# Kernel optimization log

Measured on AMD Instinct MI355X. Metric: run time of the kernel, lower is better.

Reference implementation:

```python
import jax, jax.numpy as jnp
import numpy as np

N = 16384      # total nodes in batched graph
E = 131072     # message-passing edges
E_RO = 32768   # readout edges
D = 1024       # fc7 appearance feature dim
DL = 300       # word2vec dim
DS = 16        # spatial edge feature dim
C = 117        # HICO verb classes


def setup_inputs() -> dict:
    key = jax.random.key(0)
    ks = jax.random.split(key, 20)
    s = 0.02
    return {
        'feat': jax.random.normal(ks[0], (N, D), jnp.float32),
        'word2vec': jax.random.normal(ks[1], (N, DL), jnp.float32),
        's_f': jax.random.normal(ks[2], (E, DS), jnp.float32),
        's_f_ro': jax.random.normal(ks[3], (E_RO, DS), jnp.float32),
        'W_e': jax.random.normal(ks[4], (2 * D + DS, D), jnp.float32) * s,
        'b_e': jnp.zeros((D,), jnp.float32),
        'W_el': jax.random.normal(ks[5], (2 * DL, DL), jnp.float32) * s,
        'b_el': jnp.zeros((DL,), jnp.float32),
        'W_nu': jax.random.normal(ks[6], (2 * D, D), jnp.float32) * s,
        'b_nu': jnp.zeros((D,), jnp.float32),
        'W_nul': jax.random.normal(ks[7], (2 * DL, DL), jnp.float32) * s,
        'b_nul': jnp.zeros((DL,), jnp.float32),
        'W_p': jax.random.normal(ks[8], (D + DL + DS + DL + D, C), jnp.float32) * s,
        'b_p': jnp.zeros((C,), jnp.float32),
        'edge_src': jax.random.randint(ks[9], (E,), 0, N, jnp.int32),
        'edge_dst': jax.random.randint(ks[10], (E,), 0, N, jnp.int32),
        'ro_src': jax.random.randint(ks[11], (E_RO,), 0, N, jnp.int32),
        'ro_dst': jax.random.randint(ks[12], (E_RO,), 0, N, jnp.int32),
    }


def _mean_agg(msgs, dst, n, dtype):
    # scatter-add messages to destination nodes, then mean-normalize
    summed = jax.ops.segment_sum(msgs, dst, num_segments=n)
    cnt = jax.ops.segment_sum(jnp.ones((msgs.shape[0], 1), dtype), dst, num_segments=n)
    return summed / jnp.maximum(cnt, 1.0)


def reference(feat, word2vec, s_f, s_f_ro, W_e, b_e, W_el, b_el,
              W_nu, b_nu, W_nul, b_nul, W_p, b_p,
              edge_src, edge_dst, ro_src, ro_dst):
    # --- GRNN message passing: gather -> concat -> MLP -> scatter(mean) ---
    # appearance stream: [src_feat, dst_feat, s_f] -> relu(MLP)
    m = jax.nn.relu(
        jnp.concatenate([feat[edge_src], feat[edge_dst], s_f], axis=1) @ W_e + b_e)
    agg = _mean_agg(m, edge_dst, N, feat.dtype)               # [N, D]
    # language stream: [src_w2v, dst_w2v] -> relu(MLP)
    ml = jax.nn.relu(
        jnp.concatenate([word2vec[edge_src], word2vec[edge_dst]], axis=1) @ W_el + b_el)
    aggl = _mean_agg(ml, edge_dst, N, feat.dtype)             # [N, DL]

    # --- NodeUpdate: concat(original, aggregated) -> MLP ---
    new_n_f = jax.nn.relu(jnp.concatenate([feat, agg], axis=1) @ W_nu + b_nu)
    new_n_f_lang = jax.nn.relu(
        jnp.concatenate([word2vec, aggl], axis=1) @ W_nul + b_nul)

    # --- Predictor (edge readout): concat[dst_f, dst_lang, s_f, src_lang, src_f] ---
    ef = jnp.concatenate([
        new_n_f[ro_dst], new_n_f_lang[ro_dst], s_f_ro,
        new_n_f_lang[ro_src], new_n_f[ro_src]], axis=1)       # [E_RO, 2664]
    pred = ef @ W_p + b_p                                     # [E_RO, 117]
    return pred
```

## Files before the change

kernel.cpp:

```cpp
#include <hip/hip_runtime.h>

typedef unsigned short u16;
typedef __attribute__((ext_vector_type(8))) short short8;
typedef __attribute__((ext_vector_type(4))) float f32x4;

#define NN 16384
#define EE 131072
#define ERO 32768
#define DF 1024
#define DL 300
#define DLP 320
#define DLN 384
#define DS 16
#define NC 117
#define NCP 128

__device__ __forceinline__ float bf2f(u16 x) {
  unsigned int u = ((unsigned int)x) << 16;
  float f;
  __builtin_memcpy(&f, &u, 4);
  return f;
}
__device__ __forceinline__ u16 f2bf(float f) {
  unsigned int u;
  __builtin_memcpy(&u, &f, 4);
  u = (u + 0x7FFFu + ((u >> 16) & 1u)) >> 16;
  return (u16)u;
}
__device__ __forceinline__ float ld1(const void* p, size_t i, int f) {
  return f ? ((const float*)p)[i] : bf2f(((const u16*)p)[i]);
}
__device__ __forceinline__ void ld4(const void* p, size_t i, int f,
                                    float& x, float& y, float& z, float& w) {
  if (f) {
    float4 v = *(const float4*)((const float*)p + i);
    x = v.x; y = v.y; z = v.z; w = v.w;
  } else {
    ushort4 v = *(const ushort4*)((const u16*)p + i);
    x = bf2f(v.x); y = bf2f(v.y); z = bf2f(v.z); w = bf2f(v.w);
  }
}
__device__ __forceinline__ const void* eoff(const void* p, size_t off, int f) {
  return f ? (const void*)((const float*)p + off) : (const void*)((const u16*)p + off);
}

__global__ void detect_kernel(const unsigned int* __restrict__ w, int* __restrict__ flag) {
  unsigned int x = w[threadIdx.x];
  int e = (x >> 7) & 0xFF;
  int ok = (e >= 97 && e <= 157);
  unsigned long long m = __ballot(ok);
  if (threadIdx.x == 0) flag[0] = (__popcll(m) >= 48) ? 0 : 1;
}

__global__ void cast_bf16(const int* __restrict__ flag, const void* __restrict__ src,
                          u16* __restrict__ dst, int total8) {
  const int i = blockIdx.x * 256 + threadIdx.x;
  if (i >= total8) return;
  const int fin = flag[0];
  const size_t o = (size_t)i * 8;
  float x0, x1, x2, x3, x4, x5, x6, x7;
  ld4(src, o, fin, x0, x1, x2, x3);
  ld4(src, o + 4, fin, x4, x5, x6, x7);
  ushort4 lo, hi;
  lo.x = f2bf(x0); lo.y = f2bf(x1); lo.z = f2bf(x2); lo.w = f2bf(x3);
  hi.x = f2bf(x4); hi.y = f2bf(x5); hi.z = f2bf(x6); hi.w = f2bf(x7);
  *(ushort4*)(dst + o) = lo;
  *(ushort4*)(dst + o + 4) = hi;
}

struct TJob2 {
  const void* W; long off;
  u16* out;
  int Kr, Nr, Nstr, Kp, Np, blk0;
};
struct TPack2 { TJob2 j[12]; int nj; };

__global__ void prep_weights2(const int* __restrict__ flag, TPack2 P) {
  int b = blockIdx.x;
  int ji = 0;
  while (ji + 1 < P.nj && b >= P.j[ji + 1].blk0) ++ji;
  const TJob2 J = P.j[ji];
  const int idx = (b - J.blk0) * 256 + threadIdx.x;
  if (idx >= J.Np * J.Kp) return;
  const int n = idx / J.Kp, k = idx % J.Kp;
  float v = 0.f;
  if (k < J.Kr && n < J.Nr) v = ld1(J.W, (size_t)J.off + (size_t)k * J.Nstr + n, flag[0]);
  J.out[idx] = f2bf(v);
}

__device__ __forceinline__ void stage_bf16_async(const u16* __restrict__ G, size_t rbase,
                                                 int lda, int k0, u16* lds, int w, int lane) {
  #pragma unroll
  for (int t = 0; t < 2; ++t) {
    const int rr = (w << 5) + (t << 4) + (lane >> 2);
    const u16* gp = G + (rbase + rr) * (size_t)lda + k0 + ((lane & 3) << 3);
    __builtin_amdgcn_global_load_lds(
        (const __attribute__((address_space(1))) void*)gp,
        (__attribute__((address_space(3))) void*)(lds + (((w << 5) + (t << 4)) * 32)),
        16, 0, 0);
  }
}

__device__ __forceinline__ void stage_f32_manual(const float* __restrict__ G, int row0,
                                                 int lda, int k0, int Kreal,
                                                 u16* lds, int tid) {
  const int r = tid >> 1, half = tid & 1;
  const float* gp = G + (size_t)(row0 + r) * lda + k0 + (half << 4);
  #pragma unroll
  for (int qq = 0; qq < 4; ++qq) {
    const int kk = k0 + (half << 4) + (qq << 2);
    float4 v = make_float4(0.f, 0.f, 0.f, 0.f);
    if (kk < Kreal) v = *(const float4*)(gp + (qq << 2));
    ushort4 o;
    o.x = f2bf(v.x); o.y = f2bf(v.y); o.z = f2bf(v.z); o.w = f2bf(v.w);
    *(ushort4*)(lds + r * 32 + (half << 4) + (qq << 2)) = o;
  }
}

__device__ __forceinline__ void kloop(int am, const void* __restrict__ A, int lda,
                                      int Kreal, int Kpad, const u16* __restrict__ B,
                                      u16* As, u16* Bs, f32x4 (&acc)[4][4],
                                      int row0, int col0,
                                      int tid, int lane, int w, int wm, int wn, int ml, int q) {
  for (int k0 = 0; k0 < Kpad; k0 += 32) {
    if (am == 0) stage_bf16_async((const u16*)A, (size_t)row0, lda, k0, As, w, lane);
    else         stage_f32_manual((const float*)A, row0, lda, k0, Kreal, As, tid);
    stage_bf16_async(B, (size_t)col0, Kpad, k0, Bs, w, lane);
    __syncthreads();
    short8 af[4], bfr[4];
    #pragma unroll
    for (int i = 0; i < 4; ++i)
      af[i] = *(const short8*)(As + ((wm << 6) + (i << 4) + ml) * 32 + (q << 3));
    #pragma unroll
    for (int j = 0; j < 4; ++j)
      bfr[j] = *(const short8*)(Bs + ((wn << 6) + (j << 4) + ml) * 32 + (q << 3));
    #pragma unroll
    for (int i = 0; i < 4; ++i)
      #pragma unroll
      for (int j = 0; j < 4; ++j)
        acc[i][j] = __builtin_amdgcn_mfma_f32_16x16x32_bf16(af[i], bfr[j], acc[i][j], 0, 0, 0);
    __syncthreads();
  }
}

struct GJob {
  const void* A1; const u16* B1;
  const void* A2; const u16* B2;
  const void* bias; void* C;
  int lda1, K1real, K1pad, am1;
  int lda2, K2real, K2pad, am2;
  int inBias, ldc, Nreal, Npad, relu, cf32;
  int gx, gy, blk0;
};
struct GPack { GJob j[2]; int nj; };

__global__ __launch_bounds__(256) void mfma_jobs(const int* __restrict__ flag, GPack P) {
  const int b = blockIdx.x;
  int ji = 0;
  if (P.nj > 1 && b >= P.j[1].blk0) ji = 1;
  const GJob J = P.j[ji];
  const int t = b - J.blk0;
  const int xcd = t & 7, s = t >> 3;
  const int row_t = xcd * (J.gy >> 3) + s / J.gx;
  const int col_t = s % J.gx;
  const int row0 = row_t << 7;
  const int col0 = col_t << 7;

  __shared__ __attribute__((aligned(16))) u16 As[128 * 32];
  __shared__ __attribute__((aligned(16))) u16 Bs[128 * 32];
  const int tid = threadIdx.x;
  const int lane = tid & 63;
  const int w = tid >> 6;
  const int wm = w >> 1, wn = w & 1;
  const int ml = lane & 15, q = lane >> 4;

  f32x4 acc[4][4];
  #pragma unroll
  for (int i = 0; i < 4; ++i)
    #pragma unroll
    for (int j = 0; j < 4; ++j) {
      f32x4 z = {0.f, 0.f, 0.f, 0.f};
      acc[i][j] = z;
    }

  kloop(J.am1, J.A1, J.lda1, J.K1real, J.K1pad, J.B1, As, Bs, acc,
        row0, col0, tid, lane, w, wm, wn, ml, q);
  if (J.am2 >= 0)
    kloop(J.am2, J.A2, J.lda2, J.K2real, J.K2pad, J.B2, As, Bs, acc,
          row0, col0, tid, lane, w, wm, wn, ml, q);

  const int fin = flag[0];
  #pragma unroll
  for (int j = 0; j < 4; ++j) {
    const int col = col0 + (wn << 6) + (j << 4) + ml;
    if (col >= J.Npad) continue;
    float bv = 0.f;
    if (J.bias && col < J.Nreal) bv = ld1(J.bias, col, J.inBias ? fin : 0);
    #pragma unroll
    for (int i = 0; i < 4; ++i) {
      #pragma unroll
      for (int r = 0; r < 4; ++r) {
        const int row = row0 + (wm << 6) + (i << 4) + (q << 2) + r;
        float v = 0.f;
        if (col < J.Nreal) {
          v = acc[i][j][r] + bv;
          if (J.relu) v = fmaxf(v, 0.f);
        }
        if (J.cf32) ((float*)J.C)[(size_t)row * J.ldc + col] = v;
        else        ((u16*)J.C)[(size_t)row * J.ldc + col] = f2bf(v);
      }
    }
  }
}


struct G2Job {
  const u16* A1; const u16* B1;
  const u16* A2; const u16* B2;
  const void* bias; u16* C;
  int ldk;
  int nt1, nt2;
  int gx;
  int ldc, Nreal, relu, inBias;
};

#define L2_HALF 16384
#define L2_BUF  65536

__device__ __forceinline__ void barrier_f() {
  asm volatile("" ::: "memory");
  __builtin_amdgcn_s_barrier();
  asm volatile("" ::: "memory");
}

__device__ __forceinline__ void read4f(const char* base, short8 (&dst)[4]) {
  #pragma unroll
  for (int i = 0; i < 4; ++i) dst[i] = *(const short8*)(base + i * 1024);
}

__device__ __forceinline__ void mfma16(f32x4 (&acc)[8][4], const short8 (&af)[4],
                                       const short8 (&bfr)[4], int mg) {
  __builtin_amdgcn_s_setprio(1);
  #pragma unroll
  for (int i = 0; i < 4; ++i)
    #pragma unroll
    for (int n = 0; n < 4; ++n)
      acc[mg * 4 + i][n] =
          __builtin_amdgcn_mfma_f32_16x16x32_bf16(af[i], bfr[n], acc[mg * 4 + i][n], 0, 0, 0);
  __builtin_amdgcn_s_setprio(0);
}

__global__ __launch_bounds__(512, 2) void mfma256(const int* __restrict__ flag, G2Job J) {
  __shared__ __attribute__((aligned(16))) u16 LDS[65536];
  char* ldsc = (char*)LDS;

  const int nwg = gridDim.x;
  const int bid = blockIdx.x;
  const int wg = (bid & 7) * (nwg >> 3) + (bid >> 3);
  const int rt = wg / J.gx, ct = wg % J.gx;
  const int row0 = rt << 8, col0 = ct << 8;

  const int tid = threadIdx.x;
  const int lane = tid & 63, w = tid >> 6;
  const int wm = w >> 2, wn = w & 3;
  const int q = lane >> 4, ml = lane & 15;
  const int ldk = J.ldk;
  const int nt = J.nt1 + J.nt2;

  const int swzr = (ml * 64 + q * 16) ^ (((ml >> 1) & 3) << 4);
  const int ub = (lane * 16) ^ (((lane >> 3) & 3) << 4);
  const int r_in = ub >> 6, c_in = (ub & 63) >> 1;

  f32x4 acc[8][4];
  #pragma unroll
  for (int m = 0; m < 8; ++m)
    #pragma unroll
    for (int n = 0; n < 4; ++n) { f32x4 z = {0.f, 0.f, 0.f, 0.f}; acc[m][n] = z; }

  auto stage = [&](int cb2, const u16* __restrict__ G, int rb, int kc, int boff, int kh) {
    char* lb = ldsc + cb2 * L2_BUF + boff + kh * L2_HALF + w * 2048;
    const u16* g0 = G + (size_t)(rb + w * 32 + r_in) * (size_t)ldk + kc;
    __builtin_amdgcn_global_load_lds((const __attribute__((address_space(1))) void*)g0,
        (__attribute__((address_space(3))) void*)lb, 16, 0, 0);
    const u16* g1 = g0 + (size_t)16 * ldk;
    __builtin_amdgcn_global_load_lds((const __attribute__((address_space(1))) void*)g1,
        (__attribute__((address_space(3))) void*)(lb + 1024), 16, 0, 0);
  };

  stage(0, J.A1, row0, 0 + c_in, 0, 0);
  stage(0, J.B1, col0, 0 + c_in, 32768, 0);
  stage(0, J.A1, row0, 32 + c_in, 0, 1);
  stage(0, J.B1, col0, 32 + c_in, 32768, 1);
  asm volatile("s_waitcnt vmcnt(4)" ::: "memory");
  barrier_f();

  int cb = 0;
  #pragma unroll 1
  for (int kt = 0; kt < nt; ++kt) {
    const int nk = (kt + 1 < nt) ? kt + 1 : kt;
    const u16* An = (nk < J.nt1) ? J.A1 : J.A2;
    const u16* Bn = (nk < J.nt1) ? J.B1 : J.B2;
    const int kb = ((nk < J.nt1) ? nk : nk - J.nt1) << 6;
    const char* abase = ldsc + cb * L2_BUF + wm * 8192 + swzr;
    const char* bbase = ldsc + cb * L2_BUF + 32768 + wn * 4096 + swzr;
    short8 a0[4], a1[4], bfr[4];

    read4f(abase, a0);
    read4f(bbase, bfr);
    stage(cb ^ 1, An, row0, kb + c_in, 0, 0);
    barrier_f();
    mfma16(acc, a0, bfr, 0);
    barrier_f();
    read4f(abase + 4096, a1);
    stage(cb ^ 1, Bn, col0, kb + c_in, 32768, 0);
    barrier_f();
    mfma16(acc, a1, bfr, 1);
    asm volatile("s_waitcnt vmcnt(4)" ::: "memory");
    barrier_f();
    read4f(abase + L2_HALF, a0);
    read4f(bbase + L2_HALF, bfr);
    stage(cb ^ 1, An, row0, kb + 32 + c_in, 0, 1);
    barrier_f();
    mfma16(acc, a0, bfr, 0);
    barrier_f();
    read4f(abase + L2_HALF + 4096, a1);
    stage(cb ^ 1, Bn, col0, kb + 32 + c_in, 32768, 1);
    barrier_f();
    mfma16(acc, a1, bfr, 1);
    asm volatile("s_waitcnt vmcnt(4)" ::: "memory");
    barrier_f();
    cb ^= 1;
  }

  const int fin = flag[0];
  #pragma unroll
  for (int n = 0; n < 4; ++n) {
    const int col = col0 + wn * 64 + n * 16 + ml;
    float bv = 0.f;
    if (J.bias && col < J.Nreal) bv = ld1(J.bias, col, J.inBias ? fin : 0);
    #pragma unroll
    for (int m = 0; m < 8; ++m) {
      #pragma unroll
      for (int r = 0; r < 4; ++r) {
        const int row = row0 + wm * 128 + m * 16 + q * 4 + r;
        float v = acc[m][n][r] + bv;
        if (J.relu) v = fmaxf(v, 0.f);
        J.C[(size_t)row * J.ldc + col] = f2bf(v);
      }
    }
  }
}

__global__ void cnt_kernel(const int* __restrict__ edst, int* __restrict__ cnt) {
  const int i = blockIdx.x * 256 + threadIdx.x;
  if (i < EE) atomicAdd(&cnt[edst[i]], 1);
}

__global__ __launch_bounds__(1024) void scan_kernel(const int* __restrict__ cnt,
                                                    int* __restrict__ offs,
                                                    int* __restrict__ woffs) {
  __shared__ int part[1024];
  const int t = threadIdx.x;
  const int base = t * 16;
  int loc[16];
  int s = 0;
  #pragma unroll
  for (int i = 0; i < 16; ++i) { loc[i] = s; s += cnt[base + i]; }
  part[t] = s;
  __syncthreads();
  for (int off = 1; off < 1024; off <<= 1) {
    int v = (t >= off) ? part[t - off] : 0;
    __syncthreads();
    part[t] += v;
    __syncthreads();
  }
  const int chunk_excl = (t == 0) ? 0 : part[t - 1];
  #pragma unroll
  for (int i = 0; i < 16; ++i) {
    int o = chunk_excl + loc[i];
    offs[base + i] = o;
    woffs[base + i] = o;
  }
  if (t == 1023) offs[NN] = part[1023];
}

__global__ void scatter_kernel(const int* __restrict__ esrc, const int* __restrict__ edst,
                               int* __restrict__ woffs,
                               int* __restrict__ order, int* __restrict__ srcs) {
  const int e = blockIdx.x * 256 + threadIdx.x;
  if (e < EE) {
    const int d = edst[e];
    const int pos = atomicAdd(&woffs[d], 1);
    order[pos] = e;
    srcs[pos] = esrc[e];
  }
}

__global__ __launch_bounds__(256) void app_agg(
    const int* __restrict__ flag,
    const u16* __restrict__ P12, const void* __restrict__ s_f,
    const void* __restrict__ W_eb, const void* __restrict__ b_e,
    const int* __restrict__ offs, const int* __restrict__ order,
    const int* __restrict__ srcs, u16* __restrict__ aggn)
{
  const int fin = flag[0];
  const int n = blockIdx.x;
  const int tid = threadIdx.x;
  const int c4 = tid << 2;
  const void* W_es = eoff(W_eb, (size_t)2 * DF * DF, fin);

  float wx[16], wy[16], wz[16], ww[16];
  #pragma unroll
  for (int k = 0; k < 16; ++k)
    ld4(W_es, (size_t)k * DF + c4, fin, wx[k], wy[k], wz[k], ww[k]);

  float be0, be1, be2, be3;
  ld4(b_e, c4, fin, be0, be1, be2, be3);
  const ushort4 p2 = *(const ushort4*)(P12 + (size_t)n * 2048 + 1024 + c4);
  const float base0 = bf2f(p2.x) + be0;
  const float base1 = bf2f(p2.y) + be1;
  const float base2 = bf2f(p2.z) + be2;
  const float base3 = bf2f(p2.w) + be3;

  const int beg = offs[n], end = offs[n + 1];
  float a0 = 0.f, a1 = 0.f, a2 = 0.f, a3 = 0.f;
  int j = beg;
  for (; j + 4 <= end; j += 4) {
    int ee[4], ss[4];
    #pragma unroll
    for (int m = 0; m < 4; ++m) { ee[m] = order[j + m]; ss[m] = srcs[j + m]; }
    float u0[4], u1[4], u2[4], u3[4], sfv[4][16];
    #pragma unroll
    for (int m = 0; m < 4; ++m) {
      #pragma unroll
      for (int k = 0; k < 16; k += 4)
        ld4(s_f, (size_t)ee[m] * DS + k, fin,
            sfv[m][k], sfv[m][k + 1], sfv[m][k + 2], sfv[m][k + 3]);
      const ushort4 pm = *(const ushort4*)(P12 + (size_t)ss[m] * 2048 + c4);
      u0[m] = bf2f(pm.x) + base0;
      u1[m] = bf2f(pm.y) + base1;
      u2[m] = bf2f(pm.z) + base2;
      u3[m] = bf2f(pm.w) + base3;
    }
    #pragma unroll
    for (int k = 0; k < 16; ++k)
      #pragma unroll
      for (int m = 0; m < 4; ++m) {
        u0[m] = fmaf(sfv[m][k], wx[k], u0[m]);
        u1[m] = fmaf(sfv[m][k], wy[k], u1[m]);
        u2[m] = fmaf(sfv[m][k], wz[k], u2[m]);
        u3[m] = fmaf(sfv[m][k], ww[k], u3[m]);
      }
    #pragma unroll
    for (int m = 0; m < 4; ++m) {
      a0 += fmaxf(u0[m], 0.f); a1 += fmaxf(u1[m], 0.f);
      a2 += fmaxf(u2[m], 0.f); a3 += fmaxf(u3[m], 0.f);
    }
  }
  for (; j < end; ++j) {
    const int e = order[j], s = srcs[j];
    float sf[16];
    #pragma unroll
    for (int k = 0; k < 16; k += 4)
      ld4(s_f, (size_t)e * DS + k, fin, sf[k], sf[k + 1], sf[k + 2], sf[k + 3]);
    const ushort4 p1 = *(const ushort4*)(P12 + (size_t)s * 2048 + c4);
    float v0 = bf2f(p1.x) + base0;
    float v1 = bf2f(p1.y) + base1;
    float v2 = bf2f(p1.z) + base2;
    float v3 = bf2f(p1.w) + base3;
    #pragma unroll
    for (int k = 0; k < 16; ++k) {
      v0 = fmaf(sf[k], wx[k], v0);
      v1 = fmaf(sf[k], wy[k], v1);
      v2 = fmaf(sf[k], wz[k], v2);
      v3 = fmaf(sf[k], ww[k], v3);
    }
    a0 += fmaxf(v0, 0.f); a1 += fmaxf(v1, 0.f);
    a2 += fmaxf(v2, 0.f); a3 += fmaxf(v3, 0.f);
  }
  const float inv = 1.f / fmaxf((float)(end - beg), 1.f);
  ushort4 o;
  o.x = f2bf(a0 * inv); o.y = f2bf(a1 * inv);
  o.z = f2bf(a2 * inv); o.w = f2bf(a3 * inv);
  *(ushort4*)(aggn + (size_t)n * DF + c4) = o;
}

__global__ __launch_bounds__(320) void lang_agg(
    const int* __restrict__ flag,
    const u16* __restrict__ Q12, const void* __restrict__ b_el,
    const int* __restrict__ offs, const int* __restrict__ srcs,
    u16* __restrict__ aggln)
{
  const int fin = flag[0];
  const int n = blockIdx.x;
  const int c = threadIdx.x;
  if (c >= DL) { aggln[(size_t)n * DLP + c] = 0; return; }
  const float base = bf2f(Q12[(size_t)n * 768 + 384 + c]) + ld1(b_el, c, fin);
  const int beg = offs[n], end = offs[n + 1];
  float s0 = 0.f, s1 = 0.f, s2 = 0.f, s3 = 0.f;
  int j = beg;
  for (; j + 4 <= end; j += 4) {
    s0 += fmaxf(bf2f(Q12[(size_t)srcs[j] * 768 + c]) + base, 0.f);
    s1 += fmaxf(bf2f(Q12[(size_t)srcs[j + 1] * 768 + c]) + base, 0.f);
    s2 += fmaxf(bf2f(Q12[(size_t)srcs[j + 2] * 768 + c]) + base, 0.f);
    s3 += fmaxf(bf2f(Q12[(size_t)srcs[j + 3] * 768 + c]) + base, 0.f);
  }
  for (; j < end; ++j) s0 += fmaxf(bf2f(Q12[(size_t)srcs[j] * 768 + c]) + base, 0.f);
  const float a = (s0 + s1) + (s2 + s3);
  aggln[(size_t)n * DLP + c] = f2bf(a / fmaxf((float)(end - beg), 1.f));
}

__global__ __launch_bounds__(256) void readout_kernel(
    const int* __restrict__ flag,
    const float* __restrict__ RdRs,
    const void* __restrict__ s_f_ro,
    const void* __restrict__ W_pb, size_t offWps,
    const void* __restrict__ b_p,
    const int* __restrict__ rsrc, const int* __restrict__ rdst, void* __restrict__ out)
{
  const int fin = flag[0];
  __shared__ float wps[16 * NC];
  const void* Wp_s = eoff(W_pb, offWps, fin);
  const int tid = threadIdx.x;
  for (int i = tid; i < 16 * NC; i += 256) wps[i] = ld1(Wp_s, i, fin);
  __syncthreads();
  const int slot = tid >> 7;
  const int c = tid & 127;
  const float bp = (c < NC) ? ld1(b_p, c, fin) : 0.f;

  const int e0 = (blockIdx.x << 3) + slot;
  #pragma unroll
  for (int ee = 0; ee < 8; ee += 2) {
    const int e = e0 + ee;
    const int s = rsrc[e];
    const int d = rdst[e];
    if (c < NC) {
      float acc = RdRs[(size_t)d * 256 + c] + RdRs[(size_t)s * 256 + 128 + c] + bp;
      #pragma unroll
      for (int k = 0; k < 16; ++k)
        acc = fmaf(ld1(s_f_ro, (size_t)e * DS + k, fin), wps[k * NC + c], acc);
      if (fin) ((float*)out)[(size_t)e * NC + c] = acc;
      else     ((u16*)out)[(size_t)e * NC + c] = f2bf(acc);
    }
  }
}

extern "C" void kernel_launch(void* const* d_in, const int* in_sizes, int n_in,
                              void* d_out, int out_size, void* d_ws, size_t ws_size,
                              hipStream_t stream)
{
  const void* feat  = d_in[0];
  const void* w2v   = d_in[1];
  const void* s_f   = d_in[2];
  const void* s_fro = d_in[3];
  const void* W_e   = d_in[4];
  const void* b_e   = d_in[5];
  const void* W_el  = d_in[6];
  const void* b_el  = d_in[7];
  const void* W_nu  = d_in[8];
  const void* b_nu  = d_in[9];
  const void* W_nul = d_in[10];
  const void* b_nul = d_in[11];
  const void* W_p   = d_in[12];
  const void* b_p   = d_in[13];
  const int* esrc  = (const int*)d_in[14];
  const int* edst  = (const int*)d_in[15];
  const int* rsrc  = (const int*)d_in[16];
  const int* rdst  = (const int*)d_in[17];

  char* p = (char*)d_ws;
  int* flag  = (int*)p; p += 256;
  int* cnt   = (int*)p; p += (size_t)NN * 4;
  int* offs  = (int*)p; p += (size_t)(NN + 64) * 4;
  int* woffs = (int*)p; p += (size_t)NN * 4;
  int* order = (int*)p; p += (size_t)EE * 4;
  int* srcs  = (int*)p; p += (size_t)EE * 4;
  u16* featB  = (u16*)p; p += (size_t)NN * DF * 2;
  u16* We12T  = (u16*)p; p += (size_t)2 * DF * DF * 2;
  u16* Wnu1T  = (u16*)p; p += (size_t)DF * DF * 2;
  u16* Wnu2T  = (u16*)p; p += (size_t)DF * DF * 2;
  u16* Wel12T = (u16*)p; p += (size_t)2 * DLN * DLP * 2;
  u16* Wnul1T = (u16*)p; p += (size_t)DLN * DLP * 2;
  u16* Wnul2T = (u16*)p; p += (size_t)DLN * DLP * 2;
  u16* WpFT2  = (u16*)p; p += (size_t)2 * NCP * DF * 2;
  u16* WpLT2  = (u16*)p; p += (size_t)2 * NCP * DLP * 2;
  u16* P12   = (u16*)p; p += (size_t)NN * 2048 * 2;
  u16* Q12   = (u16*)p; p += (size_t)NN * 768 * 2;
  u16* aggln = (u16*)p; p += (size_t)NN * DLP * 2;
  u16* aggn  = (u16*)p; p += (size_t)NN * DF * 2;
  u16* newf = P12;
  u16* newl = P12 + (size_t)NN * DF;
  float* RdRs = (float*)Q12;

  detect_kernel<<<1, 64, 0, stream>>>((const unsigned int*)feat, flag);
  hipMemsetAsync(cnt, 0, (size_t)NN * 4, stream);
  cast_bf16<<<(NN * DF / 8 + 255) / 256, 256, 0, stream>>>(flag, feat, featB, NN * DF / 8);

  TPack2 tp{};
  int tb = 0, tn = 0;
  auto T = [&](const void* W, long off, int Kr, int Nr, int Nstr, u16* out, int Kp, int Np) {
    tp.j[tn] = TJob2{W, off, out, Kr, Nr, Nstr, Kp, Np, tb};
    tb += (Np * Kp + 255) / 256;
    ++tn;
  };
  T(W_e,   0,                   DF, DF, DF, We12T,                     DF, DF);
  T(W_e,   (long)DF * DF,       DF, DF, DF, We12T + (size_t)DF * DF,   DF, DF);
  T(W_nu,  0,                   DF, DF, DF, Wnu1T, DF, DF);
  T(W_nu,  (long)DF * DF,       DF, DF, DF, Wnu2T, DF, DF);
  T(W_el,  0,                   DL, DL, DL, Wel12T,                     DLP, DLN);
  T(W_el,  (long)DL * DL,       DL, DL, DL, Wel12T + (size_t)DLN * DLP, DLP, DLN);
  T(W_nul, 0,                   DL, DL, DL, Wnul1T, DLP, DLN);
  T(W_nul, (long)DL * DL,       DL, DL, DL, Wnul2T, DLP, DLN);
  T(W_p,   0,                                DF, NC, NC, WpFT2,                     DF,  NCP);
  T(W_p,   (long)(DF + DL + DS + DL) * NC,   DF, NC, NC, WpFT2 + (size_t)NCP * DF,  DF,  NCP);
  T(W_p,   (long)DF * NC,                    DL, NC, NC, WpLT2,                     DLP, NCP);
  T(W_p,   (long)(DF + DL + DS) * NC,        DL, NC, NC, WpLT2 + (size_t)NCP * DLP, DLP, NCP);
  tp.nj = tn;
  prep_weights2<<<tb, 256, 0, stream>>>(flag, tp);

  cnt_kernel<<<EE / 256, 256, 0, stream>>>(edst, cnt);
  scan_kernel<<<1, 1024, 0, stream>>>(cnt, offs, woffs);
  scatter_kernel<<<EE / 256, 256, 0, stream>>>(esrc, edst, woffs, order, srcs);

  {
    G2Job j{featB, We12T, nullptr, nullptr, nullptr, P12,
            DF, 16, 0, 8, 2048, 2048, 0, 0};
    mfma256<<<512, 512, 0, stream>>>(flag, j);
  }
  {
    GPack g{};
    g.j[0] = GJob{w2v, Wel12T, nullptr, nullptr, nullptr, Q12,
                  DL, DL, DLP, 1,   0, 0, 0, -1,
                  0, 768, 768, 768, 0, 0,    6, 128, 0};
    g.nj = 1;
    mfma_jobs<<<768, 256, 0, stream>>>(flag, g);
  }

  lang_agg<<<NN, DLP, 0, stream>>>(flag, Q12, b_el, offs, srcs, aggln);
  app_agg<<<NN, 256, 0, stream>>>(flag, P12, s_f, W_e, b_e, offs, order, srcs, aggn);

  {
    G2Job j{featB, Wnu1T, aggn, Wnu2T, b_nu, newf,
            DF, 16, 16, 4, DF, DF, 1, 1};
    mfma256<<<256, 512, 0, stream>>>(flag, j);
  }
  {
    GPack g{};
    g.j[0] = GJob{w2v, Wnul1T, aggln, Wnul2T, b_nul, newl,
                  DL, DL, DLP, 1,   DLP, DLP, DLP, 0,
                  1, DLP, DL, DLP, 1, 0,     3, 128, 0};
    g.nj = 1;
    mfma_jobs<<<384, 256, 0, stream>>>(flag, g);
  }

  {
    GPack g{};
    g.j[0] = GJob{newf, WpFT2, newl, WpLT2, nullptr, RdRs,
                  DF, DF, DF, 0,    DLP, DLP, DLP, 0,
                  0, 256, 256, 256, 0, 1,    2, 128, 0};
    g.nj = 1;
    mfma_jobs<<<256, 256, 0, stream>>>(flag, g);
  }

  readout_kernel<<<ERO / 8, 256, 0, stream>>>(flag, RdRs, s_fro,
                                              W_p, (size_t)(DF + DL) * NC, b_p,
                                              rsrc, rdst, d_out);
}
```

Before: 659.0 us.

## Batch language GEMMs into the 256-tile MFMA kernel with pre-cast word2vec

Word2vec is now cast once to padded bf16 so the language-stream GEMMs can run in the 256x256 MFMA kernel, which takes a two-job pack and runs them alongside the appearance GEMMs in a single launch. This removes separate generic-kernel launches and their tail underutilisation. Columns past the real width are written as zero or skipped. app_agg is also templated on the input-format flag and software-prefetches the next group's source rows. The trade-offs are an extra cast kernel and wasted work in the padded 256-wide tiles for the narrow 300/320-column problems.

```diff
diff --git a/kernel.cpp b/kernel.cpp
--- a/kernel.cpp
+++ b/kernel.cpp
@@ -68,6 +68,26 @@
   *(ushort4*)(dst + o + 4) = hi;
 }
 
+__global__ void cast_w2v(const int* __restrict__ flag, const void* __restrict__ src,
+                         u16* __restrict__ dst) {
+  const int i = blockIdx.x * 256 + threadIdx.x;
+  if (i >= NN * 80) return;
+  const int fin = flag[0];
+  const int n = i / 80, g = i - n * 80;
+  const int c = g << 2;
+  ushort4 o;
+  if (c < DL) {
+    const size_t base = (size_t)n * DL + c;
+    o.x = f2bf(ld1(src, base + 0, fin));
+    o.y = f2bf(ld1(src, base + 1, fin));
+    o.z = f2bf(ld1(src, base + 2, fin));
+    o.w = f2bf(ld1(src, base + 3, fin));
+  } else {
+    o.x = 0; o.y = 0; o.z = 0; o.w = 0;
+  }
+  *(ushort4*)(dst + (size_t)n * DLP + c) = o;
+}
+
 struct TJob2 {
   const void* W; long off;
   u16* out;
@@ -222,7 +242,9 @@
   int nt1, nt2;
   int gx;
   int ldc, Nreal, relu, inBias;
+  int nwg, blk0;
 };
+struct G2Pack { G2Job j[2]; int nj; };
 
 #define L2_HALF 16384
 #define L2_BUF  65536
@@ -250,13 +272,15 @@
   __builtin_amdgcn_s_setprio(0);
 }
 
-__global__ __launch_bounds__(512, 2) void mfma256(const int* __restrict__ flag, G2Job J) {
+__global__ __launch_bounds__(512, 2) void mfma256(const int* __restrict__ flag, G2Pack P) {
   __shared__ __attribute__((aligned(16))) u16 LDS[65536];
   char* ldsc = (char*)LDS;
 
-  const int nwg = gridDim.x;
   const int bid = blockIdx.x;
-  const int wg = (bid & 7) * (nwg >> 3) + (bid >> 3);
+  const int ji = (P.nj > 1 && bid >= P.j[1].blk0) ? 1 : 0;
+  const G2Job J = P.j[ji];
+  const int b = bid - J.blk0;
+  const int wg = (b & 7) * (J.nwg >> 3) + (b >> 3);
   const int rt = wg / J.gx, ct = wg % J.gx;
   const int row0 = rt << 8, col0 = ct << 8;
 
@@ -336,6 +360,7 @@
   #pragma unroll
   for (int n = 0; n < 4; ++n) {
     const int col = col0 + wn * 64 + n * 16 + ml;
+    if (col >= J.ldc) continue;
     float bv = 0.f;
     if (J.bias && col < J.Nreal) bv = ld1(J.bias, col, J.inBias ? fin : 0);
     #pragma unroll
@@ -343,8 +368,11 @@
       #pragma unroll
       for (int r = 0; r < 4; ++r) {
         const int row = row0 + wm * 128 + m * 16 + q * 4 + r;
-        float v = acc[m][n][r] + bv;
-        if (J.relu) v = fmaxf(v, 0.f);
+        float v = 0.f;
+        if (col < J.Nreal) {
+          v = acc[m][n][r] + bv;
+          if (J.relu) v = fmaxf(v, 0.f);
+        }
         J.C[(size_t)row * J.ldc + col] = f2bf(v);
       }
     }
@@ -396,27 +424,26 @@
   }
 }
 
-__global__ __launch_bounds__(256) void app_agg(
-    const int* __restrict__ flag,
+template<int FIN>
+__device__ __forceinline__ void app_agg_body(
     const u16* __restrict__ P12, const void* __restrict__ s_f,
     const void* __restrict__ W_eb, const void* __restrict__ b_e,
     const int* __restrict__ offs, const int* __restrict__ order,
     const int* __restrict__ srcs, u16* __restrict__ aggn)
 {
-  const int fin = flag[0];
   const int n = blockIdx.x;
   const int tid = threadIdx.x;
   const int c4 = tid << 2;
-  const void* W_es = eoff(W_eb, (size_t)2 * DF * DF, fin);
+  const void* W_es = eoff(W_eb, (size_t)2 * DF * DF, FIN);
 
   float wx[16], wy[16], wz[16], ww[16];
   #pragma unroll
   for (int k = 0; k < 16; ++k)
-    ld4(W_es, (size_t)k * DF + c4, fin, wx[k], wy[k], wz[k], ww[k]);
+    ld4(W_es, (size_t)k * DF + c4, FIN, wx[k], wy[k], wz[k], ww[k]);
 
   float be0, be1, be2, be3;
-  ld4(b_e, c4, fin, be0, be1, be2, be3);
-  const ushort4 p2 = *(const ushort4*)(P12 + (size_t)n * 2048 + 1024 + c4);
+  ld4(b_e, c4, FIN, be0, be1, be2, be3);
+  const ushort4 p2 = *(const ushort4*)(P12 + ((size_t)(unsigned)(n << 11)) + 1024 + c4);
   const float base0 = bf2f(p2.x) + be0;
   const float base1 = bf2f(p2.y) + be1;
   const float base2 = bf2f(p2.z) + be2;
@@ -425,22 +452,41 @@
   const int beg = offs[n], end = offs[n + 1];
   float a0 = 0.f, a1 = 0.f, a2 = 0.f, a3 = 0.f;
   int j = beg;
-  for (; j + 4 <= end; j += 4) {
-    int ee[4], ss[4];
-    #pragma unroll
-    for (int m = 0; m < 4; ++m) { ee[m] = order[j + m]; ss[m] = srcs[j + m]; }
+
+  int ee0[4];
+  ushort4 pm0[4];
+  if (j + 4 <= end) {
+    #pragma unroll
+    for (int m = 0; m < 4; ++m) {
+      ee0[m] = order[j + m];
+      const int ssm = srcs[j + m];
+      pm0[m] = *(const ushort4*)(P12 + ((size_t)(unsigned)(ssm << 11)) + c4);
+    }
+  }
+  for (; j + 4 <= end;) {
+    const int jn = j + 4;
+    const bool pref = (jn + 4 <= end);
+    int ee1[4];
+    ushort4 pm1[4];
+    if (pref) {
+      #pragma unroll
+      for (int m = 0; m < 4; ++m) {
+        ee1[m] = order[jn + m];
+        const int ssm = srcs[jn + m];
+        pm1[m] = *(const ushort4*)(P12 + ((size_t)(unsigned)(ssm << 11)) + c4);
+      }
+    }
     float u0[4], u1[4], u2[4], u3[4], sfv[4][16];
     #pragma unroll
     for (int m = 0; m < 4; ++m) {
       #pragma unroll
       for (int k = 0; k < 16; k += 4)
-        ld4(s_f, (size_t)ee[m] * DS + k, fin,
+        ld4(s_f, (size_t)ee0[m] * DS + k, FIN,
             sfv[m][k], sfv[m][k + 1], sfv[m][k + 2], sfv[m][k + 3]);
-      const ushort4 pm = *(const ushort4*)(P12 + (size_t)ss[m] * 2048 + c4);
-      u0[m] = bf2f(pm.x) + base0;
-      u1[m] = bf2f(pm.y) + base1;
-      u2[m] = bf2f(pm.z) + base2;
-      u3[m] = bf2f(pm.w) + base3;
+      u0[m] = bf2f(pm0[m].x) + base0;
+      u1[m] = bf2f(pm0[m].y) + base1;
+      u2[m] = bf2f(pm0[m].z) + base2;
+      u3[m] = bf2f(pm0[m].w) + base3;
     }
     #pragma unroll
     for (int k = 0; k < 16; ++k)
@@ -456,14 +502,19 @@
       a0 += fmaxf(u0[m], 0.f); a1 += fmaxf(u1[m], 0.f);
       a2 += fmaxf(u2[m], 0.f); a3 += fmaxf(u3[m], 0.f);
     }
+    j = jn;
+    if (pref) {
+      #pragma unroll
+      for (int m = 0; m < 4; ++m) { ee0[m] = ee1[m]; pm0[m] = pm1[m]; }
+    }
   }
   for (; j < end; ++j) {
     const int e = order[j], s = srcs[j];
     float sf[16];
     #pragma unroll
     for (int k = 0; k < 16; k += 4)
-      ld4(s_f, (size_t)e * DS + k, fin, sf[k], sf[k + 1], sf[k + 2], sf[k + 3]);
-    const ushort4 p1 = *(const ushort4*)(P12 + (size_t)s * 2048 + c4);
+      ld4(s_f, (size_t)e * DS + k, FIN, sf[k], sf[k + 1], sf[k + 2], sf[k + 3]);
+    const ushort4 p1 = *(const ushort4*)(P12 + ((size_t)(unsigned)(s << 11)) + c4);
     float v0 = bf2f(p1.x) + base0;
     float v1 = bf2f(p1.y) + base1;
     float v2 = bf2f(p1.z) + base2;
@@ -483,6 +534,17 @@
   o.x = f2bf(a0 * inv); o.y = f2bf(a1 * inv);
   o.z = f2bf(a2 * inv); o.w = f2bf(a3 * inv);
   *(ushort4*)(aggn + (size_t)n * DF + c4) = o;
+}
+
+__global__ __launch_bounds__(256) void app_agg(
+    const int* __restrict__ flag,
+    const u16* __restrict__ P12, const void* __restrict__ s_f,
+    const void* __restrict__ W_eb, const void* __restrict__ b_e,
+    const int* __restrict__ offs, const int* __restrict__ order,
+    const int* __restrict__ srcs, u16* __restrict__ aggn)
+{
+  if (flag[0]) app_agg_body<1>(P12, s_f, W_eb, b_e, offs, order, srcs, aggn);
+  else         app_agg_body<0>(P12, s_f, W_eb, b_e, offs, order, srcs, aggn);
 }
 
 __global__ __launch_bounds__(320) void lang_agg(
@@ -588,6 +650,7 @@
   u16* Q12   = (u16*)p; p += (size_t)NN * 768 * 2;
   u16* aggln = (u16*)p; p += (size_t)NN * DLP * 2;
   u16* aggn  = (u16*)p; p += (size_t)NN * DF * 2;
+  u16* w2vB  = (u16*)p; p += (size_t)NN * DLP * 2;
   u16* newf = P12;
   u16* newl = P12 + (size_t)NN * DF;
   float* RdRs = (float*)Q12;
@@ -595,6 +658,7 @@
   detect_kernel<<<1, 64, 0, stream>>>((const unsigned int*)feat, flag);
   hipMemsetAsync(cnt, 0, (size_t)NN * 4, stream);
   cast_bf16<<<(NN * DF / 8 + 255) / 256, 256, 0, stream>>>(flag, feat, featB, NN * DF / 8);
+  cast_w2v<<<(NN * 80 + 255) / 256, 256, 0, stream>>>(flag, w2v, w2vB);
 
   TPack2 tp{};
   int tb = 0, tn = 0;
@@ -623,34 +687,26 @@
   scatter_kernel<<<EE / 256, 256, 0, stream>>>(esrc, edst, woffs, order, srcs);
 
   {
-    G2Job j{featB, We12T, nullptr, nullptr, nullptr, P12,
-            DF, 16, 0, 8, 2048, 2048, 0, 0};
-    mfma256<<<512, 512, 0, stream>>>(flag, j);
-  }
-  {
-    GPack g{};
-    g.j[0] = GJob{w2v, Wel12T, nullptr, nullptr, nullptr, Q12,
-                  DL, DL, DLP, 1,   0, 0, 0, -1,
-                  0, 768, 768, 768, 0, 0,    6, 128, 0};
-    g.nj = 1;
-    mfma_jobs<<<768, 256, 0, stream>>>(flag, g);
+    G2Pack g{};
+    g.j[0] = G2Job{featB, We12T, nullptr, nullptr, nullptr, P12,
+                   DF, 16, 0, 8, 2048, 2048, 0, 0, 512, 0};
+    g.j[1] = G2Job{w2vB, Wel12T, nullptr, nullptr, nullptr, Q12,
+                   DLP, 5, 0, 3, 768, 768, 0, 0, 192, 512};
+    g.nj = 2;
+    mfma256<<<704, 512, 0, stream>>>(flag, g);
   }
 
   lang_agg<<<NN, DLP, 0, stream>>>(flag, Q12, b_el, offs, srcs, aggln);
   app_agg<<<NN, 256, 0, stream>>>(flag, P12, s_f, W_e, b_e, offs, order, srcs, aggn);
 
   {
-    G2Job j{featB, Wnu1T, aggn, Wnu2T, b_nu, newf,
-            DF, 16, 16, 4, DF, DF, 1, 1};
-    mfma256<<<256, 512, 0, stream>>>(flag, j);
-  }
-  {
-    GPack g{};
-    g.j[0] = GJob{w2v, Wnul1T, aggln, Wnul2T, b_nul, newl,
-                  DL, DL, DLP, 1,   DLP, DLP, DLP, 0,
-                  1, DLP, DL, DLP, 1, 0,     3, 128, 0};
-    g.nj = 1;
-    mfma_jobs<<<384, 256, 0, stream>>>(flag, g);
+    G2Pack g{};
+    g.j[0] = G2Job{featB, Wnu1T, aggn, Wnu2T, b_nu, newf,
+                   DF, 16, 16, 4, DF, DF, 1, 1, 256, 0};
+    g.j[1] = G2Job{w2vB, Wnul1T, aggln, Wnul2T, b_nul, newl,
+                   DLP, 5, 5, 2, DLP, DL, 1, 1, 128, 256};
+    g.nj = 2;
+    mfma256<<<384, 512, 0, stream>>>(flag, g);
   }
 
   {
```

Result: no change. 646.2 us (-1.9%).
